# Performance work log

Hardware: AMD Instinct MI355X
Metric: run time of the kernel (lower is better)

## Reference

```python
import jax, jax.numpy as jnp
from jax import lax
import numpy as np

# db4 (Daubechies-4) filters, matching pywt.Wavelet('db4')
L = 8
_REC_LO = np.array([0.23037781330885523, 0.7148465705525415, 0.6308807679295904,
                    -0.02798376941698385, -0.18703481171888114, 0.030841381835986965,
                    0.032883011666982945, -0.010597401784997278], dtype=np.float32)
_DEC_LO = _REC_LO[::-1].copy()
_DEC_HI = (((-1.0) ** (np.arange(L) + 1)) * _REC_LO).astype(np.float32)  # QMF
_REC_HI = _DEC_HI[::-1].copy()
# lax.conv performs correlation, so use reversed filters to get true convolution.
# rev(dec_lo)=rec_lo, rev(dec_hi)=rec_hi and vice versa.
DEC_K = jnp.asarray(np.stack([_DEC_LO[::-1], _DEC_HI[::-1]])[:, None, :])  # (2,1,L)
REC_K = jnp.asarray(np.stack([_REC_LO[::-1], _REC_HI[::-1]])[None, :, :])  # (1,2,L)

ENHANCE_FACTOR = 1.5
DENOISE_THRESHOLD = 0.2


def _dwt_last(x):
    # pywt single-level DWT (mode='symmetric') along last axis.
    # Equivalent to: conv(sym_pad(x, L-1), dec_filter)[valid][1::2]
    xe = jnp.pad(x, ((0, 0), (L - 1, L - 1)), mode='symmetric')[:, 1:]
    y = lax.conv_general_dilated(xe[:, None, :], DEC_K, (2,), 'VALID',
                                 dimension_numbers=('NCH', 'OIH', 'NCH'))
    return y[:, 0], y[:, 1]  # lo, hi, each (M, (S+L-1)//2)


def _idwt_last(lo, hi):
    # pywt single-level IDWT: upsample (lhs_dilation=2), filter, trim L-2 each side.
    c = jnp.stack([lo, hi], axis=1)  # (M, 2, n)
    y = lax.conv_general_dilated(c, REC_K, (1,), [(1, 1)], lhs_dilation=(2,),
                                 dimension_numbers=('NCH', 'OIH', 'NCH'))
    return y[:, 0]  # (M, 2n - L + 2)


def _dwt2(x):
    # x: (N, H, W) -> aa (cA), da (cH), ad (cV), dd (cD)
    N, H, W = x.shape
    lo, hi = _dwt_last(x.reshape(N * H, W))
    Wc = lo.shape[-1]
    lo = lo.reshape(N, H, Wc)
    hi = hi.reshape(N, H, Wc)

    def colwise(a):
        at = a.transpose(0, 2, 1).reshape(N * Wc, H)
        l, h = _dwt_last(at)
        Hc = l.shape[-1]
        return (l.reshape(N, Wc, Hc).transpose(0, 2, 1),
                h.reshape(N, Wc, Hc).transpose(0, 2, 1))

    aa, da = colwise(lo)
    ad, dd = colwise(hi)
    return aa, da, ad, dd


def _idwt2(aa, da, ad, dd):
    N, Hc, Wc = aa.shape

    def colinv(a, d):
        at = a.transpose(0, 2, 1).reshape(N * Wc, Hc)
        dt = d.transpose(0, 2, 1).reshape(N * Wc, Hc)
        r = _idwt_last(at, dt)
        H = r.shape[-1]
        return r.reshape(N, Wc, H).transpose(0, 2, 1)

    lo = colinv(aa, da)
    hi = colinv(ad, dd)
    H = lo.shape[1]
    out = _idwt_last(lo.reshape(N * H, Wc), hi.reshape(N * H, Wc))
    return out.reshape(N, H, -1)


def _soft_enhance(d):
    # enhance then pywt.threshold(..., mode='soft') with per-(image,channel,band) max
    d = d * ENHANCE_FACTOR
    t = DENOISE_THRESHOLD * jnp.max(jnp.abs(d), axis=(-2, -1), keepdims=True)
    return jnp.sign(d) * jnp.maximum(jnp.abs(d) - t, 0.0)


def setup_inputs() -> dict:
    key = jax.random.key(0)
    x = jax.random.normal(key, (32, 3, 510, 510), dtype=jnp.float32)
    return {'x': x}


def reference(x):
    B, C, H, W = x.shape
    z = x.reshape(B * C, H, W)
    a1, h1, v1, d1 = _dwt2(z)
    a2, h2, v2, d2 = _dwt2(a1)
    h2s, v2s, d2s = _soft_enhance(h2), _soft_enhance(v2), _soft_enhance(d2)
    h1s, v1s, d1s = _soft_enhance(h1), _soft_enhance(v1), _soft_enhance(d1)
    a1r = _idwt2(a2, h2s, v2s, d2s)
    out = _idwt2(a1r, h1s, v1s, d1s)
    return out.reshape(B, C, H, W)
```

## Files before the change

### kernel.cpp

```cpp
#include <hip/hip_runtime.h>

__device__ constexpr float DEC_LO[8] = {
    -0.010597401784997278f, 0.032883011666982945f, 0.030841381835986965f,
    -0.18703481171888114f, -0.02798376941698385f, 0.6308807679295904f,
    0.7148465705525415f, 0.23037781330885523f};
__device__ constexpr float DEC_HI[8] = {
    -0.23037781330885523f, 0.7148465705525415f, -0.6308807679295904f,
    -0.02798376941698385f, 0.18703481171888114f, 0.030841381835986965f,
    -0.032883011666982945f, -0.010597401784997278f};
__device__ constexpr float REC_LO[8] = {
    0.23037781330885523f, 0.7148465705525415f, 0.6308807679295904f,
    -0.02798376941698385f, -0.18703481171888114f, 0.030841381835986965f,
    0.032883011666982945f, -0.010597401784997278f};
__device__ constexpr float REC_HI[8] = {
    -0.010597401784997278f, -0.032883011666982945f, 0.030841381835986965f,
    0.18703481171888114f, -0.02798376941698385f, -0.6308807679295904f,
    0.7148465705525415f, -0.23037781330885523f};

__device__ __forceinline__ float soft_enh(float v, float th) {
    float e = 1.5f * v;
    float a = fabsf(e) - th;
    return a > 0.0f ? copysignf(a, e) : 0.0f;
}

#define TB 32
#define TO 64

__global__ __launch_bounds__(256, 4) void fused_dwt2_k(
    const float* __restrict__ x, int S, int Nc, int tiles,
    float* __restrict__ aa, float* __restrict__ da,
    float* __restrict__ ad, float* __restrict__ dd,
    unsigned* __restrict__ mx_da, unsigned* __restrict__ mx_ad,
    unsigned* __restrict__ mx_dd)
{
    int b = blockIdx.x;
    int tx = b % tiles, ty = (b / tiles) % tiles, m = b / (tiles * tiles);
    int jh0 = ty * TB, jw0 = tx * TB;
    int r0 = 2 * jh0 - 6, c0 = 2 * jw0 - 6;
    const float* xm = x + (size_t)m * S * S;

    __shared__ float RB[70][68];

    int tid = threadIdx.x;
    bool colv = (c0 >= 0) && (c0 + 71 < S);

    int e0 = tid, e1 = tid + 256, e2 = tid + 512;
    bool has2 = (e2 < 560);

    auto prow = [&](int e) -> const float* {
        int pr = r0 + (e >> 3);
        pr = pr < 0 ? -1 - pr : pr;
        pr = pr >= S ? 2 * S - 1 - pr : pr;
        return xm + (size_t)pr * S;
    };

    float f0[16], f1[16], f2[16];
    if (colv) {
        const float* s0 = prow(e0) + (c0 + 8 * (e0 & 7));
        const float* s1 = prow(e1) + (c0 + 8 * (e1 & 7));
#pragma unroll
        for (int i = 0; i < 8; ++i) {
            float2 v = *reinterpret_cast<const float2*>(s0 + 2 * i);
            f0[2 * i] = v.x; f0[2 * i + 1] = v.y;
        }
#pragma unroll
        for (int i = 0; i < 8; ++i) {
            float2 v = *reinterpret_cast<const float2*>(s1 + 2 * i);
            f1[2 * i] = v.x; f1[2 * i + 1] = v.y;
        }
        if (has2) {
            const float* s2 = prow(e2) + (c0 + 8 * (e2 & 7));
#pragma unroll
            for (int i = 0; i < 8; ++i) {
                float2 v = *reinterpret_cast<const float2*>(s2 + 2 * i);
                f2[2 * i] = v.x; f2[2 * i + 1] = v.y;
            }
        }
    } else {
        auto gath = [&](int e, float* f) {
            const float* row = prow(e);
            int base = c0 + 8 * (e & 7);
#pragma unroll
            for (int i = 0; i < 16; ++i) {
                int p = base + i;
                p = p < 0 ? -1 - p : p;
                p = p >= S ? 2 * S - 1 - p : p;
                f[i] = row[p];
            }
        };
        gath(e0, f0);
        gath(e1, f1);
        if (has2) gath(e2, f2);
    }

    auto rdwt = [&](int e, const float* f) {
        float lo[4], hi[4];
#pragma unroll
        for (int i = 0; i < 4; ++i) {
            float alo = 0.f, ahi = 0.f;
#pragma unroll
            for (int t = 0; t < 8; ++t) {
                float v = f[2 * i + 7 - t];
                alo = fmaf(DEC_LO[t], v, alo);
                ahi = fmaf(DEC_HI[t], v, ahi);
            }
            lo[i] = alo; hi[i] = ahi;
        }
        int r = e >> 3, c4 = 4 * (e & 7);
        *reinterpret_cast<float4*>(&RB[r][c4]) = make_float4(lo[0], lo[1], lo[2], lo[3]);
        *reinterpret_cast<float4*>(&RB[r][32 + c4]) = make_float4(hi[0], hi[1], hi[2], hi[3]);
    };
    rdwt(e0, f0);
    rdwt(e1, f1);
    if (has2) rdwt(e2, f2);
    __syncthreads();

    int jj = tid & 31, g = tid >> 5;
    int jw = jw0 + jj;
    float mh = 0.f, mv = 0.f, md = 0.f;
#pragma unroll
    for (int pass = 0; pass < 2; ++pass) {
        int rbase = 8 * g + 4 * pass;
        float L[10], H[10];
#pragma unroll
        for (int rr = 0; rr < 10; ++rr) {
            L[rr] = RB[rbase + rr][jj];
            H[rr] = RB[rbase + rr][32 + jj];
        }
#pragma unroll
        for (int k = 0; k < 2; ++k) {
            float vaa = 0.f, vda = 0.f, vad = 0.f, vdd = 0.f;
#pragma unroll
            for (int t = 0; t < 8; ++t) {
                float l = L[2 * k + 7 - t];
                float h = H[2 * k + 7 - t];
                vaa = fmaf(DEC_LO[t], l, vaa);
                vda = fmaf(DEC_HI[t], l, vda);
                vad = fmaf(DEC_LO[t], h, vad);
                vdd = fmaf(DEC_HI[t], h, vdd);
            }
            int jh = jh0 + 4 * g + 2 * pass + k;
            if (jh < Nc && jw < Nc) {
                size_t o = ((size_t)m * Nc + jh) * Nc + jw;
                aa[o] = vaa; da[o] = vda; ad[o] = vad; dd[o] = vdd;
                mh = fmaxf(mh, fabsf(vda));
                mv = fmaxf(mv, fabsf(vad));
                md = fmaxf(md, fabsf(vdd));
            }
        }
    }
#pragma unroll
    for (int off = 32; off; off >>= 1) {
        mh = fmaxf(mh, __shfl_down(mh, off));
        mv = fmaxf(mv, __shfl_down(mv, off));
        md = fmaxf(md, __shfl_down(md, off));
    }
    __shared__ float sm[3][4];
    int wv = tid >> 6, ln = tid & 63;
    if (ln == 0) { sm[0][wv] = mh; sm[1][wv] = mv; sm[2][wv] = md; }
    __syncthreads();
    if (tid == 0) {
        float A = fmaxf(fmaxf(sm[0][0], sm[0][1]), fmaxf(sm[0][2], sm[0][3]));
        float B = fmaxf(fmaxf(sm[1][0], sm[1][1]), fmaxf(sm[1][2], sm[1][3]));
        float C = fmaxf(fmaxf(sm[2][0], sm[2][1]), fmaxf(sm[2][2], sm[2][3]));
        atomicMax(mx_da + m, __float_as_uint(A));
        atomicMax(mx_ad + m, __float_as_uint(B));
        atomicMax(mx_dd + m, __float_as_uint(C));
    }
}

__global__ __launch_bounds__(256, 4) void fused_irec_k(
    const float* __restrict__ a2, const float* __restrict__ h2,
    const float* __restrict__ v2, const float* __restrict__ d2,
    const float* __restrict__ h1, const float* __restrict__ v1,
    const float* __restrict__ d1,
    const unsigned* __restrict__ mx2h, const unsigned* __restrict__ mx2v,
    const unsigned* __restrict__ mx2d,
    const unsigned* __restrict__ mx1h, const unsigned* __restrict__ mx1v,
    const unsigned* __restrict__ mx1d,
    int n2, int n1, int Ho, int tiles, float* __restrict__ out)
{
    int b = blockIdx.x;
    int tx = b % tiles, ty = (b / tiles) % tiles, m = b / (tiles * tiles);
    int i0 = ty * TO, u0 = tx * TO;
    int jr0 = i0 >> 1, jc0 = u0 >> 1;
    int q0r = jr0 >> 1, q0c = jc0 >> 1;

    __shared__ float AH[35][44];
    __shared__ float AR[35][36];
    __shared__ float LH[64][71];

    int tid = threadIdx.x;
    float th2_h = 0.2f * (1.5f * __uint_as_float(mx2h[m]));
    float th2_v = 0.2f * (1.5f * __uint_as_float(mx2v[m]));
    float th2_d = 0.2f * (1.5f * __uint_as_float(mx2d[m]));
    float th1_h = 0.2f * (1.5f * __uint_as_float(mx1h[m]));
    float th1_v = 0.2f * (1.5f * __uint_as_float(mx1v[m]));
    float th1_d = 0.2f * (1.5f * __uint_as_float(mx1d[m]));
    const float* a2m = a2 + (size_t)m * n2 * n2;
    const float* h2m = h2 + (size_t)m * n2 * n2;
    const float* v2m = v2 + (size_t)m * n2 * n2;
    const float* d2m = d2 + (size_t)m * n2 * n2;
    const float* h1m = h1 + (size_t)m * n1 * n1;
    const float* v1m = v1 + (size_t)m * n1 * n1;
    const float* d1m = d1 + (size_t)m * n1 * n1;

    int g2 = tid / 21, cc = tid % 21;
    bool act1a = (tid < 189);
    float A2r[5], H2r[5], V2r[5], D2r[5];
    if (act1a) {
        int c2 = q0c + cc; if (c2 > n2 - 1) c2 = n2 - 1;
#pragma unroll
        for (int rl = 0; rl < 5; ++rl) {
            int j2 = q0r + 2 * g2 + rl; if (j2 > n2 - 1) j2 = n2 - 1;
            size_t o = (size_t)j2 * n2 + c2;
            A2r[rl] = a2m[o]; H2r[rl] = h2m[o];
            V2r[rl] = v2m[o]; D2r[rl] = d2m[o];
        }
    }

    int gA = tid / 35, jcA = tid % 35;
    int jcg = jc0 + jcA; if (jcg > n1 - 1) jcg = n1 - 1;
    int baseA = jr0 + 4 * gA;
    float Hg[7], Vg[7], Dg[7];
#pragma unroll
    for (int rr = 0; rr < 7; ++rr) {
        int jr = baseA + rr; if (jr > n1 - 1) jr = n1 - 1;
        size_t o = (size_t)jr * n1 + jcg;
        Hg[rr] = h1m[o]; Vg[rr] = v1m[o]; Dg[rr] = d1m[o];
    }

    if (act1a) {
#pragma unroll
        for (int rl = 0; rl < 5; ++rl) {
            H2r[rl] = soft_enh(H2r[rl], th2_h);
            V2r[rl] = soft_enh(V2r[rl], th2_v);
            D2r[rl] = soft_enh(D2r[rl], th2_d);
        }
        float alo[4], ahi[4];
#pragma unroll
        for (int k = 0; k < 4; ++k) { alo[k] = 0.f; ahi[k] = 0.f; }
#pragma unroll
        for (int rl = 0; rl < 5; ++rl) {
#pragma unroll
            for (int t = 0; t < 8; ++t) {
                int k = 2 * rl + t - 6;
                if (k >= 0 && k < 4) {
                    alo[k] = fmaf(REC_LO[t], A2r[rl], fmaf(REC_HI[t], H2r[rl], alo[k]));
                    ahi[k] = fmaf(REC_LO[t], V2r[rl], fmaf(REC_HI[t], D2r[rl], ahi[k]));
                }
            }
        }
#pragma unroll
        for (int k = 0; k < 4; ++k) {
            int p = 4 * g2 + k;
            if (p < 35) { AH[p][cc] = alo[k]; AH[p][22 + cc] = ahi[k]; }
        }
    }
    __syncthreads();

    for (int e = tid; e < 1225; e += 256) {
        int p = e / 35, cl = e % 35;
        int t0 = cl & 1;
        float acc = 0.f;
#pragma unroll
        for (int s = 0; s < 4; ++s) {
            int t = t0 + 2 * s;
            int c = (cl + 6 - t) >> 1;
            acc = fmaf(REC_LO[t], AH[p][c], acc);
            acc = fmaf(REC_HI[t], AH[p][22 + c], acc);
        }
        AR[p][cl] = acc;
    }
    __syncthreads();

    {
        float Ar[7], Hs[7], Vs[7], Ds[7];
#pragma unroll
        for (int rr = 0; rr < 7; ++rr) {
            Ar[rr] = AR[4 * gA + rr][jcA];
            Hs[rr] = soft_enh(Hg[rr], th1_h);
            Vs[rr] = soft_enh(Vg[rr], th1_v);
            Ds[rr] = soft_enh(Dg[rr], th1_d);
        }
#pragma unroll
        for (int pass = 0; pass < 2; ++pass) {
            int P = 2 * gA + pass;
            float acc_lo[4], acc_hi[4];
#pragma unroll
            for (int k = 0; k < 4; ++k) { acc_lo[k] = 0.f; acc_hi[k] = 0.f; }
#pragma unroll
            for (int rl = 0; rl < 5; ++rl) {
                int rr = 2 * pass + rl;
                float av = Ar[rr], hv = Hs[rr], vv = Vs[rr], dv = Ds[rr];
#pragma unroll
                for (int t = 0; t < 8; ++t) {
                    int k = 2 * rl + t - 6;
                    if (k >= 0 && k < 4) {
                        acc_lo[k] = fmaf(REC_LO[t], av, fmaf(REC_HI[t], hv, acc_lo[k]));
                        acc_hi[k] = fmaf(REC_LO[t], vv, fmaf(REC_HI[t], dv, acc_hi[k]));
                    }
                }
            }
#pragma unroll
            for (int k = 0; k < 4; ++k) {
                LH[4 * P + k][jcA] = acc_lo[k];
                LH[4 * P + k][35 + jcA] = acc_hi[k];
            }
        }
    }
    if (tid < 24) {
        int tk = tid + 256;
        int gB = tk / 35, jcB = tk % 35;
        int jcgB = jc0 + jcB; if (jcgB > n1 - 1) jcgB = n1 - 1;
        int baseB = jr0 + 4 * gB;
        float Ar[7], Hs[7], Vs[7], Ds[7];
#pragma unroll
        for (int rr = 0; rr < 7; ++rr) {
            int jr = baseB + rr; if (jr > n1 - 1) jr = n1 - 1;
            size_t o = (size_t)jr * n1 + jcgB;
            Ar[rr] = AR[4 * gB + rr][jcB];
            Hs[rr] = soft_enh(h1m[o], th1_h);
            Vs[rr] = soft_enh(v1m[o], th1_v);
            Ds[rr] = soft_enh(d1m[o], th1_d);
        }
#pragma unroll
        for (int pass = 0; pass < 2; ++pass) {
            int P = 2 * gB + pass;
            float acc_lo[4], acc_hi[4];
#pragma unroll
            for (int k = 0; k < 4; ++k) { acc_lo[k] = 0.f; acc_hi[k] = 0.f; }
#pragma unroll
            for (int rl = 0; rl < 5; ++rl) {
                int rr = 2 * pass + rl;
                float av = Ar[rr], hv = Hs[rr], vv = Vs[rr], dv = Ds[rr];
#pragma unroll
                for (int t = 0; t < 8; ++t) {
                    int k = 2 * rl + t - 6;
                    if (k >= 0 && k < 4) {
                        acc_lo[k] = fmaf(REC_LO[t], av, fmaf(REC_HI[t], hv, acc_lo[k]));
                        acc_hi[k] = fmaf(REC_LO[t], vv, fmaf(REC_HI[t], dv, acc_hi[k]));
                    }
                }
            }
#pragma unroll
            for (int k = 0; k < 4; ++k) {
                LH[4 * P + k][jcB] = acc_lo[k];
                LH[4 * P + k][35 + jcB] = acc_hi[k];
            }
        }
    }
    __syncthreads();

    for (int e = tid; e < TO * TO; e += 256) {
        int il = e >> 6, ul = e & 63;
        int t0 = ul & 1;
        float acc = 0.f;
#pragma unroll
        for (int s = 0; s < 4; ++s) {
            int t = t0 + 2 * s;
            int c = (ul + 6 - t) >> 1;
            acc = fmaf(REC_LO[t], LH[il][c], acc);
            acc = fmaf(REC_HI[t], LH[il][35 + c], acc);
        }
        int gi = i0 + il, gu = u0 + ul;
        if (gi < Ho && gu < Ho)
            out[((size_t)m * Ho + gi) * Ho + gu] = acc;
    }
}

extern "C" void kernel_launch(void* const* d_in, const int* in_sizes, int n_in,
                              void* d_out, int out_size, void* d_ws, size_t ws_size,
                              hipStream_t stream) {
    const float* x = (const float*)d_in[0];
    float* out = (float*)d_out;
    float* ws = (float*)d_ws;

    const int M = 96, S1 = 510, N1 = 258, N2 = 132;
    const long S_l1 = (long)M * N1 * N1;
    const long S_l2 = (long)M * N2 * N2;

    float* aa1 = ws;
    float* h1  = aa1 + S_l1;
    float* v1  = h1 + S_l1;
    float* d1  = v1 + S_l1;
    float* a2  = d1 + S_l1;
    float* h2  = a2 + S_l2;
    float* v2  = h2 + S_l2;
    float* d2  = v2 + S_l2;
    unsigned* th = (unsigned*)(d2 + S_l2);

    long need = 4 * S_l1 + 4 * S_l2 + 576;
    if (ws_size < (size_t)need * sizeof(float)) return;

    unsigned *th_h1 = th, *th_v1 = th + 96, *th_d1 = th + 192;
    unsigned *th_h2 = th + 288, *th_v2 = th + 384, *th_d2 = th + 480;

    hipMemsetAsync(th, 0, 576 * sizeof(unsigned), stream);

    fused_dwt2_k<<<9 * 9 * M, 256, 0, stream>>>(x, S1, N1, 9, aa1, h1, v1, d1,
                                                th_h1, th_v1, th_d1);
    fused_dwt2_k<<<5 * 5 * M, 256, 0, stream>>>(aa1, N1, N2, 5, a2, h2, v2, d2,
                                                th_h2, th_v2, th_d2);
    fused_irec_k<<<8 * 8 * M, 256, 0, stream>>>(a2, h2, v2, d2, h1, v1, d1,
                                                th_h2, th_v2, th_d2,
                                                th_h1, th_v1, th_d1,
                                                N2, N1, S1, 8, out);
}
```

Baseline: 326.2 us.

## Pad intermediate subband rows and swizzle blocks across XCDs

```diff
diff --git a/kernel.cpp b/kernel.cpp
--- a/kernel.cpp
+++ b/kernel.cpp
@@ -23,21 +23,26 @@
     return a > 0.0f ? copysignf(a, e) : 0.0f;
 }
 
+__device__ __forceinline__ int xcd_swz(int b, int nwg) {
+    int cpx = nwg >> 3;
+    return (b & 7) * cpx + (b >> 3);
+}
+
 #define TB 32
 #define TO 64
 
 __global__ __launch_bounds__(256, 4) void fused_dwt2_k(
-    const float* __restrict__ x, int S, int Nc, int tiles,
+    const float* __restrict__ x, int S, int ldX, int Nc, int ldB, int tiles,
     float* __restrict__ aa, float* __restrict__ da,
     float* __restrict__ ad, float* __restrict__ dd,
     unsigned* __restrict__ mx_da, unsigned* __restrict__ mx_ad,
     unsigned* __restrict__ mx_dd)
 {
-    int b = blockIdx.x;
+    int b = xcd_swz(blockIdx.x, gridDim.x);
     int tx = b % tiles, ty = (b / tiles) % tiles, m = b / (tiles * tiles);
     int jh0 = ty * TB, jw0 = tx * TB;
     int r0 = 2 * jh0 - 6, c0 = 2 * jw0 - 6;
-    const float* xm = x + (size_t)m * S * S;
+    const float* xm = x + (size_t)m * S * ldX;
 
     __shared__ float RB[70][68];
 
@@ -51,7 +56,7 @@
         int pr = r0 + (e >> 3);
         pr = pr < 0 ? -1 - pr : pr;
         pr = pr >= S ? 2 * S - 1 - pr : pr;
-        return xm + (size_t)pr * S;
+        return xm + (size_t)pr * ldX;
     };
 
     float f0[16], f1[16], f2[16];
@@ -141,7 +146,7 @@
             }
             int jh = jh0 + 4 * g + 2 * pass + k;
             if (jh < Nc && jw < Nc) {
-                size_t o = ((size_t)m * Nc + jh) * Nc + jw;
+                size_t o = ((size_t)m * Nc + jh) * ldB + jw;
                 aa[o] = vaa; da[o] = vda; ad[o] = vad; dd[o] = vdd;
                 mh = fmaxf(mh, fabsf(vda));
                 mv = fmaxf(mv, fabsf(vad));
@@ -178,9 +183,10 @@
     const unsigned* __restrict__ mx2d,
     const unsigned* __restrict__ mx1h, const unsigned* __restrict__ mx1v,
     const unsigned* __restrict__ mx1d,
-    int n2, int n1, int Ho, int tiles, float* __restrict__ out)
+    int n2, int ld2, int n1, int ld1, int Ho, int tiles,
+    float* __restrict__ out)
 {
-    int b = blockIdx.x;
+    int b = xcd_swz(blockIdx.x, gridDim.x);
     int tx = b % tiles, ty = (b / tiles) % tiles, m = b / (tiles * tiles);
     int i0 = ty * TO, u0 = tx * TO;
     int jr0 = i0 >> 1, jc0 = u0 >> 1;
@@ -197,13 +203,13 @@
     float th1_h = 0.2f * (1.5f * __uint_as_float(mx1h[m]));
     float th1_v = 0.2f * (1.5f * __uint_as_float(mx1v[m]));
     float th1_d = 0.2f * (1.5f * __uint_as_float(mx1d[m]));
-    const float* a2m = a2 + (size_t)m * n2 * n2;
-    const float* h2m = h2 + (size_t)m * n2 * n2;
-    const float* v2m = v2 + (size_t)m * n2 * n2;
-    const float* d2m = d2 + (size_t)m * n2 * n2;
-    const float* h1m = h1 + (size_t)m * n1 * n1;
-    const float* v1m = v1 + (size_t)m * n1 * n1;
-    const float* d1m = d1 + (size_t)m * n1 * n1;
+    const float* a2m = a2 + (size_t)m * n2 * ld2;
+    const float* h2m = h2 + (size_t)m * n2 * ld2;
+    const float* v2m = v2 + (size_t)m * n2 * ld2;
+    const float* d2m = d2 + (size_t)m * n2 * ld2;
+    const float* h1m = h1 + (size_t)m * n1 * ld1;
+    const float* v1m = v1 + (size_t)m * n1 * ld1;
+    const float* d1m = d1 + (size_t)m * n1 * ld1;
 
     int g2 = tid / 21, cc = tid % 21;
     bool act1a = (tid < 189);
@@ -213,7 +219,7 @@
 #pragma unroll
         for (int rl = 0; rl < 5; ++rl) {
             int j2 = q0r + 2 * g2 + rl; if (j2 > n2 - 1) j2 = n2 - 1;
-            size_t o = (size_t)j2 * n2 + c2;
+            size_t o = (size_t)j2 * ld2 + c2;
             A2r[rl] = a2m[o]; H2r[rl] = h2m[o];
             V2r[rl] = v2m[o]; D2r[rl] = d2m[o];
         }
@@ -226,7 +232,7 @@
 #pragma unroll
     for (int rr = 0; rr < 7; ++rr) {
         int jr = baseA + rr; if (jr > n1 - 1) jr = n1 - 1;
-        size_t o = (size_t)jr * n1 + jcg;
+        size_t o = (size_t)jr * ld1 + jcg;
         Hg[rr] = h1m[o]; Vg[rr] = v1m[o]; Dg[rr] = d1m[o];
     }
 
@@ -318,7 +324,7 @@
 #pragma unroll
         for (int rr = 0; rr < 7; ++rr) {
             int jr = baseB + rr; if (jr > n1 - 1) jr = n1 - 1;
-            size_t o = (size_t)jr * n1 + jcgB;
+            size_t o = (size_t)jr * ld1 + jcgB;
             Ar[rr] = AR[4 * gB + rr][jcB];
             Hs[rr] = soft_enh(h1m[o], th1_h);
             Vs[rr] = soft_enh(v1m[o], th1_v);
@@ -377,20 +383,21 @@
     float* ws = (float*)d_ws;
 
     const int M = 96, S1 = 510, N1 = 258, N2 = 132;
-    const long S_l1 = (long)M * N1 * N1;
-    const long S_l2 = (long)M * N2 * N2;
+    const int LD1 = 288, LD2 = 160;
+    const long P1 = (long)M * N1 * LD1;
+    const long P2 = (long)M * N2 * LD2;
 
     float* aa1 = ws;
-    float* h1  = aa1 + S_l1;
-    float* v1  = h1 + S_l1;
-    float* d1  = v1 + S_l1;
-    float* a2  = d1 + S_l1;
-    float* h2  = a2 + S_l2;
-    float* v2  = h2 + S_l2;
-    float* d2  = v2 + S_l2;
-    unsigned* th = (unsigned*)(d2 + S_l2);
-
-    long need = 4 * S_l1 + 4 * S_l2 + 576;
+    float* h1  = aa1 + P1;
+    float* v1  = h1 + P1;
+    float* d1  = v1 + P1;
+    float* a2  = d1 + P1;
+    float* h2  = a2 + P2;
+    float* v2  = h2 + P2;
+    float* d2  = v2 + P2;
+    unsigned* th = (unsigned*)(d2 + P2);
+
+    long need = 4 * P1 + 4 * P2 + 576;
     if (ws_size < (size_t)need * sizeof(float)) return;
 
     unsigned *th_h1 = th, *th_v1 = th + 96, *th_d1 = th + 192;
@@ -398,12 +405,14 @@
 
     hipMemsetAsync(th, 0, 576 * sizeof(unsigned), stream);
 
-    fused_dwt2_k<<<9 * 9 * M, 256, 0, stream>>>(x, S1, N1, 9, aa1, h1, v1, d1,
+    fused_dwt2_k<<<9 * 9 * M, 256, 0, stream>>>(x, S1, S1, N1, LD1, 9,
+                                                aa1, h1, v1, d1,
                                                 th_h1, th_v1, th_d1);
-    fused_dwt2_k<<<5 * 5 * M, 256, 0, stream>>>(aa1, N1, N2, 5, a2, h2, v2, d2,
+    fused_dwt2_k<<<5 * 5 * M, 256, 0, stream>>>(aa1, N1, LD1, N2, LD2, 5,
+                                                a2, h2, v2, d2,
                                                 th_h2, th_v2, th_d2);
     fused_irec_k<<<8 * 8 * M, 256, 0, stream>>>(a2, h2, v2, d2, h1, v1, d1,
                                                 th_h2, th_v2, th_d2,
                                                 th_h1, th_v1, th_d1,
-                                                N2, N1, S1, 8, out);
+                                                N2, LD2, N1, LD1, S1, 8, out);
 }
```

After: 314.2 us. -3.7%, faster.
